# Kernel optimization log

Measured on AMD Instinct MI355X. Metric: run time of the kernel, lower is better.

Reference implementation:

```python
import jax, jax.numpy as jnp
import numpy as np

CUTOFF = 5.0
N_ATOMS = 1024
CELL_SIZE = 30.0  # Angstrom-scale cubic-ish cell


def setup_inputs() -> dict:
    key = jax.random.key(0)
    k1, k2 = jax.random.split(key)
    # fractional coordinates in [0, 1)
    frac = jax.random.uniform(k1, (N_ATOMS, 3), dtype=jnp.float32)
    # slightly perturbed cubic lattice cell (rows are lattice vectors)
    cell = CELL_SIZE * jnp.eye(3, dtype=jnp.float32) \
        + 0.5 * jax.random.normal(k2, (3, 3), dtype=jnp.float32)
    return {"frac": frac, "cell": cell}


def reference(frac, cell):
    """Periodic radius graph via minimum-image over the 27 neighbor cells.

    Returns dist_masked [N, N, 27]: Cartesian pair distance d(i, j, image k)
    where the pair is an edge (0 < d < CUTOFF), else 0. Nonzero entries are
    exactly the edges of the periodic radius graph with their distances.
    """
    # 27 integer image offsets in {-1,0,1}^3 -> [27, 3]
    g = jnp.arange(-1.0, 2.0, dtype=frac.dtype)
    offsets = jnp.stack(jnp.meshgrid(g, g, g, indexing="ij"), axis=-1).reshape(27, 3)

    # fractional displacement frac[j] - frac[i] + offset  -> [N, N, 27, 3]
    dfrac = frac[None, :, None, :] - frac[:, None, None, :] + offsets[None, None, :, :]
    # to Cartesian: row-vector convention, r = f @ cell
    vec = jnp.einsum("ijkd,de->ijke", dfrac, cell)

    d2 = jnp.sum(vec * vec, axis=-1)  # [N, N, 27]
    # safe sqrt: avoid nan grads at exact-zero (self, zero-image) pairs
    dist = jnp.where(d2 > 0.0, jnp.sqrt(jnp.where(d2 > 0.0, d2, 1.0)), 0.0)

    mask = (d2 > 1e-12) & (dist < CUTOFF)  # excludes self pair at zero offset
    return dist * mask
```

## Files before the change

kernel.cpp:

```cpp
#include <hip/hip_runtime.h>


#define NATOMS 1024
#define NIMG 27
#define CUTOFF_F 5.0f
#define TOTAL (NATOMS * NATOMS * NIMG)

__global__ __launch_bounds__(256) void PeriodicRadiusGraph_kernel(
    const float* __restrict__ frac,
    const float* __restrict__ cell,
    float* __restrict__ out)
{
    unsigned idx = blockIdx.x * 256u + threadIdx.x;

    unsigned k = idx % 27u;
    unsigned t = idx / 27u;
    unsigned j = t & (NATOMS - 1u);
    unsigned i = t >> 10;

    float c00 = cell[0], c01 = cell[1], c02 = cell[2];
    float c10 = cell[3], c11 = cell[4], c12 = cell[5];
    float c20 = cell[6], c21 = cell[7], c22 = cell[8];

    float ox = (float)((int)(k / 9u) - 1);
    float oy = (float)((int)((k / 3u) % 3u) - 1);
    float oz = (float)((int)(k % 3u) - 1);

    float fx = frac[3u * j + 0u] - frac[3u * i + 0u] + ox;
    float fy = frac[3u * j + 1u] - frac[3u * i + 1u] + oy;
    float fz = frac[3u * j + 2u] - frac[3u * i + 2u] + oz;

    float vx = fx * c00 + fy * c10 + fz * c20;
    float vy = fx * c01 + fy * c11 + fz * c21;
    float vz = fx * c02 + fy * c12 + fz * c22;

    float d2 = vx * vx + vy * vy + vz * vz;
    float d  = sqrtf(d2);
    float r  = (d2 > 1e-12f && d < CUTOFF_F) ? d : 0.0f;

    out[idx] = r;
}

extern "C" void kernel_launch(void* const* d_in, const int* in_sizes, int n_in,
                              void* d_out, int out_size, void* d_ws, size_t ws_size,
                              hipStream_t stream) {
    const float* frac = (const float*)d_in[0];
    const float* cell = (const float*)d_in[1];
    float* out = (float*)d_out;

    const int block = 256;
    const int grid = TOTAL / block;
    PeriodicRadiusGraph_kernel<<<grid, block, 0, stream>>>(frac, cell, out);
}
```

Baseline: 142.4 us.

## Compute all 27 images per pair and stage through shared memory for float4 stores

Each thread now handles one atom pair and loops over all 27 image offsets, so the per-element divide by 27 and the repeated loads of frac and cell go away. Results are written into a shared-memory tile and then copied to global memory as coalesced float4 stores. In exchange the kernel uses about 27 KB of shared memory per block, which can lower occupancy, and it adds a block barrier.

After: 120.8 us. 1.18x faster.

```diff
diff --git a/kernel.cpp b/kernel.cpp
--- a/kernel.cpp
+++ b/kernel.cpp
@@ -4,41 +4,63 @@
 #define NATOMS 1024
 #define NIMG 27
 #define CUTOFF_F 5.0f
-#define TOTAL (NATOMS * NATOMS * NIMG)
+#define PAIRS_PER_BLOCK 256
+#define FLOATS_PER_BLOCK (PAIRS_PER_BLOCK * NIMG)
+#define VEC4_PER_BLOCK (FLOATS_PER_BLOCK / 4)
 
 __global__ __launch_bounds__(256) void PeriodicRadiusGraph_kernel(
     const float* __restrict__ frac,
     const float* __restrict__ cell,
     float* __restrict__ out)
 {
-    unsigned idx = blockIdx.x * 256u + threadIdx.x;
+    __shared__ float tile[FLOATS_PER_BLOCK];
 
-    unsigned k = idx % 27u;
-    unsigned t = idx / 27u;
-    unsigned j = t & (NATOMS - 1u);
-    unsigned i = t >> 10;
+    const unsigned t = threadIdx.x;
+    const unsigned q = blockIdx.x * PAIRS_PER_BLOCK + t;
+    const unsigned j = q & (NATOMS - 1u);
+    const unsigned i = q >> 10;
 
-    float c00 = cell[0], c01 = cell[1], c02 = cell[2];
-    float c10 = cell[3], c11 = cell[4], c12 = cell[5];
-    float c20 = cell[6], c21 = cell[7], c22 = cell[8];
+    const float c00 = cell[0], c01 = cell[1], c02 = cell[2];
+    const float c10 = cell[3], c11 = cell[4], c12 = cell[5];
+    const float c20 = cell[6], c21 = cell[7], c22 = cell[8];
 
-    float ox = (float)((int)(k / 9u) - 1);
-    float oy = (float)((int)((k / 3u) % 3u) - 1);
-    float oz = (float)((int)(k % 3u) - 1);
+    const float fix = frac[3u * i + 0u], fiy = frac[3u * i + 1u], fiz = frac[3u * i + 2u];
+    const float fjx = frac[3u * j + 0u], fjy = frac[3u * j + 1u], fjz = frac[3u * j + 2u];
 
-    float fx = frac[3u * j + 0u] - frac[3u * i + 0u] + ox;
-    float fy = frac[3u * j + 1u] - frac[3u * i + 1u] + oy;
-    float fz = frac[3u * j + 2u] - frac[3u * i + 2u] + oz;
+    const float dfx = fjx - fix;
+    const float dfy = fjy - fiy;
+    const float dfz = fjz - fiz;
 
-    float vx = fx * c00 + fy * c10 + fz * c20;
-    float vy = fx * c01 + fy * c11 + fz * c21;
-    float vz = fx * c02 + fy * c12 + fz * c22;
+    float* row = &tile[t * NIMG];
 
-    float d2 = vx * vx + vy * vy + vz * vz;
-    float d  = sqrtf(d2);
-    float r  = (d2 > 1e-12f && d < CUTOFF_F) ? d : 0.0f;
+#pragma unroll
+    for (int k = 0; k < NIMG; ++k) {
+        const float ox = (float)(k / 9 - 1);
+        const float oy = (float)((k / 3) % 3 - 1);
+        const float oz = (float)(k % 3 - 1);
 
-    out[idx] = r;
+        const float fx = dfx + ox;
+        const float fy = dfy + oy;
+        const float fz = dfz + oz;
+
+        const float vx = fx * c00 + fy * c10 + fz * c20;
+        const float vy = fx * c01 + fy * c11 + fz * c21;
+        const float vz = fx * c02 + fy * c12 + fz * c22;
+
+        const float d2 = vx * vx + vy * vy + vz * vz;
+        const float d  = sqrtf(d2);
+        row[k] = (d2 > 1e-12f && d < CUTOFF_F) ? d : 0.0f;
+    }
+
+    __syncthreads();
+
+    float4* out4 = (float4*)(out + (size_t)blockIdx.x * FLOATS_PER_BLOCK);
+    const float4* tile4 = (const float4*)tile;
+#pragma unroll
+    for (int c = 0; c < 7; ++c) {
+        const int l = c * 256 + (int)t;
+        if (l < VEC4_PER_BLOCK) out4[l] = tile4[l];
+    }
 }
 
 extern "C" void kernel_launch(void* const* d_in, const int* in_sizes, int n_in,
@@ -48,7 +70,6 @@
     const float* cell = (const float*)d_in[1];
     float* out = (float*)d_out;
 
-    const int block = 256;
-    const int grid = TOTAL / block;
-    PeriodicRadiusGraph_kernel<<<grid, block, 0, stream>>>(frac, cell, out);
+    const int grid = (NATOMS * NATOMS) / PAIRS_PER_BLOCK;
+    PeriodicRadiusGraph_kernel<<<grid, PAIRS_PER_BLOCK, 0, stream>>>(frac, cell, out);
 }
```
